# Performance work log

Hardware: AMD Instinct MI355X
Metric: run time of the kernel (lower is better)

Reference implementation:

```python
import jax, jax.numpy as jnp
import numpy as np

N_NODES = 100000
N_EDGES = 3200000
N_IN = 128
N_OUT = 64
ITERATIONS = 150
LEAK = 0.01


def _mml_activation(v):
    # piecewise: leaky below 0, Michaelis-Menten-like saturation above 0.5
    v = jnp.where(v < 0, v * LEAK, v)
    safe = jnp.where(v > 0.5, v, 1.0)  # avoid div-by-zero on untaken branch
    return jnp.where(v > 0.5, 1.0 - 0.25 / safe, v)


def setup_inputs() -> dict:
    key = jax.random.key(0)
    ks = jax.random.split(key, 9)
    x = jax.random.normal(ks[0], (1, N_IN), dtype=jnp.float32)
    in_weights = jnp.ones((N_IN,), jnp.float32)  # inputAmplitude * ones
    # weights init: 0.1 + 0.1*U, sign flipped for inhibitory reactions
    mag = 0.1 + 0.1 * jax.random.uniform(ks[1], (N_EDGES,), dtype=jnp.float32)
    sign = jnp.where(jax.random.bernoulli(ks[2], 0.5, (N_EDGES,)), 1.0, -1.0)
    rec_weights = mag * sign
    biases = 0.001 * jnp.ones((N_NODES,), jnp.float32)
    out_weights = jnp.ones((N_OUT,), jnp.float32)  # projectionAmplitude * ones
    in_indices = jax.random.randint(ks[3], (N_IN,), 0, N_NODES, dtype=jnp.int32)
    edge_rows = jax.random.randint(ks[4], (N_EDGES,), 0, N_NODES, dtype=jnp.int32)
    edge_cols = jax.random.randint(ks[5], (N_EDGES,), 0, N_NODES, dtype=jnp.int32)
    out_indices = jax.random.randint(ks[6], (N_OUT,), 0, N_NODES, dtype=jnp.int32)
    return {"x": x, "in_weights": in_weights, "rec_weights": rec_weights,
            "biases": biases, "out_weights": out_weights,
            "in_indices": in_indices, "edge_rows": edge_rows,
            "edge_cols": edge_cols, "out_indices": out_indices}


def reference(x, in_weights, rec_weights, biases, out_weights,
              in_indices, edge_rows, edge_cols, out_indices):
    # input projection: scatter weighted inputs into node vector [N_NODES]
    node_in = jnp.zeros((N_NODES,), x.dtype).at[in_indices].set(in_weights * x[0])
    b_in = node_in + biases

    def step(y, _):
        # sparse matvec A @ y: gather sources, weight, scatter-add to rows
        s = jax.ops.segment_sum(rec_weights * y[edge_cols], edge_rows,
                                num_segments=N_NODES)
        return _mml_activation(s + b_in), None

    y0 = jnp.zeros((N_NODES,), x.dtype)
    y, _ = jax.lax.scan(step, y0, None, length=ITERATIONS)
    # output projection: gather + scale -> [1, N_OUT]
    return (out_weights * y[out_indices])[None, :]
```

## Files before the change

kernel.cpp:

```cpp
#include <hip/hip_runtime.h>

#define N_NODES 100000
#define N_EDGES 3200000
#define N_IN    128
#define N_OUT   64
#define ITERS   150
#define LEAK    0.01f

#define NT      960
#define GROUPS  240
#define NBW     255
#define GRID    256
#define RPB2    393
#define NCH     9
#define CH      11520
#define CHF4    2880
#define NKEYS   (NCH * N_NODES)
#define SCAN_CHUNK 1024
#define SCAN_NBLK  879
#define NEPC    16
#define EPST    32
#define YSTR    (NCH * CH)

__device__ __forceinline__ float mml(float v) {
    v = (v < 0.0f) ? v * LEAK : v;
    if (v > 0.5f) v = 1.0f - 0.25f / v;
    return v;
}

__global__ void k_binit(const float* __restrict__ biases, float* __restrict__ b_in) {
    int i = blockIdx.x * blockDim.x + threadIdx.x;
    if (i < N_NODES) b_in[i] = biases[i];
}

__global__ void k_scatter_in(const float* __restrict__ x,
                             const float* __restrict__ in_w,
                             const int*   __restrict__ in_idx,
                             const float* __restrict__ biases,
                             float* __restrict__ b_in) {
    int k = threadIdx.x;
    if (k < N_IN) {
        int idx = in_idx[k];
        bool last = true;
        for (int j = k + 1; j < N_IN; ++j)
            if (in_idx[j] == idx) { last = false; break; }
        if (last) b_in[idx] = biases[idx] + in_w[k] * x[k];
    }
}

__global__ void k_y0(const float* __restrict__ b_in, float* __restrict__ y0) {
    int i = blockIdx.x * blockDim.x + threadIdx.x;
    if (i < N_NODES) y0[i] = mml(b_in[i]);
}

__global__ void k_hist(const int* __restrict__ rows, const int* __restrict__ cols,
                       int* __restrict__ counts) {
    int i = blockIdx.x * blockDim.x + threadIdx.x;
    int stride = gridDim.x * blockDim.x;
    for (; i < N_EDGES; i += stride) {
        int key = (cols[i] / CH) * N_NODES + rows[i];
        atomicAdd(&counts[key], 1);
    }
}

__global__ void k_scan1(const int* __restrict__ counts, int* __restrict__ rp,
                        int* __restrict__ blockSums) {
    __shared__ int sm[SCAN_CHUNK];
    int t = threadIdx.x;
    int i = blockIdx.x * SCAN_CHUNK + t;
    int v = (i < NKEYS) ? counts[i] : 0;
    sm[t] = v;
    __syncthreads();
    for (int off = 1; off < SCAN_CHUNK; off <<= 1) {
        int add = (t >= off) ? sm[t - off] : 0;
        __syncthreads();
        sm[t] += add;
        __syncthreads();
    }
    if (i <= NKEYS) rp[i] = sm[t] - v;
    if (t == SCAN_CHUNK - 1) blockSums[blockIdx.x] = sm[t];
}

__global__ void k_scan2(int* __restrict__ blockSums) {
    __shared__ int sm[1024];
    int t = threadIdx.x;
    int v = (t < SCAN_NBLK) ? blockSums[t] : 0;
    sm[t] = v;
    __syncthreads();
    for (int off = 1; off < 1024; off <<= 1) {
        int add = (t >= off) ? sm[t - off] : 0;
        __syncthreads();
        sm[t] += add;
        __syncthreads();
    }
    if (t < SCAN_NBLK) blockSums[t] = sm[t] - v;
}

__global__ void k_scan3(int* __restrict__ rp, const int* __restrict__ blockSums,
                        int* __restrict__ next) {
    int i = blockIdx.x * SCAN_CHUNK + threadIdx.x;
    if (i <= NKEYS) {
        int val = rp[i] + blockSums[blockIdx.x];
        rp[i] = val;
        if (i < NKEYS) next[i] = val;
    }
}

__global__ void k_scatter_edges(const int* __restrict__ rows, const int* __restrict__ cols,
                                const float* __restrict__ w,
                                int* __restrict__ next, int2* __restrict__ csr) {
    int i = blockIdx.x * blockDim.x + threadIdx.x;
    int stride = gridDim.x * blockDim.x;
    for (; i < N_EDGES; i += stride) {
        int c = cols[i];
        int g = c / CH;
        int key = g * N_NODES + rows[i];
        int p = atomicAdd(&next[key], 1);
        csr[p] = make_int2(c - g * CH, __float_as_int(w[i]));
    }
}

__device__ __forceinline__ void stage_chunk(const float* __restrict__ src,
                                            float* __restrict__ dst_lds,
                                            int t, int sc1mode) {
    if (!sc1mode) {
        #pragma unroll
        for (int i = 0; i < 3; ++i) {
            const int f4 = i * NT + t;
            __builtin_amdgcn_global_load_lds(
                (const __attribute__((address_space(1))) void*)(src + (size_t)f4 * 4),
                (__attribute__((address_space(3))) void*)(dst_lds + (size_t)f4 * 4),
                16, 0, 0);
        }
    } else {
        for (int i = t; i < CH; i += NT)
            dst_lds[i] = __hip_atomic_load(&src[i], __ATOMIC_RELAXED,
                                           __HIP_MEMORY_SCOPE_AGENT);
        asm volatile("s_waitcnt lgkmcnt(0)" ::: "memory");
    }
}

__device__ __forceinline__ void gate_poll(const int* __restrict__ epoch,
                                          int c, int need, int b) {
    while (__hip_atomic_load(&epoch[(c * NEPC + (b & (NEPC - 1))) * EPST],
                             __ATOMIC_RELAXED, __HIP_MEMORY_SCOPE_AGENT) < need)
        __builtin_amdgcn_s_sleep(1);
}

__global__ __launch_bounds__(NT) void k_iterate(
    const int*  __restrict__ rp2,
    const int2* __restrict__ csr,
    const float* __restrict__ b_in,
    float* __restrict__ ybufs,
    int* __restrict__ arr,
    int* __restrict__ epoch,
    const int* __restrict__ out_idx,
    const float* __restrict__ out_w,
    float* __restrict__ out,
    int nbuf, int sc1mode)
{
    __shared__ float sbufA[CH], sbufB[CH];
    __shared__ int   s_rp[NCH * 400];
    const int b = blockIdx.x, t = threadIdx.x;

    if (b == 0) {
        if (t < NCH * 64) {
            const int c = t >> 6, k = t & 63;
            int cend = (c + 1) * CH; if (cend > N_NODES) cend = N_NODES;
            const int wf = (c * CH) / RPB2;
            const int wl = (cend - 1) / RPB2;
            const int sz = wl - wf + 1;
            for (int v = 1; v <= ITERS - 1; ++v) {
                if (k < sz) {
                    while (__hip_atomic_load(&arr[1 + wf + k], __ATOMIC_RELAXED,
                                             __HIP_MEMORY_SCOPE_AGENT) < v)
                        __builtin_amdgcn_s_sleep(2);
                }
                if (k < NEPC)
                    __hip_atomic_store(&epoch[(c * NEPC + k) * EPST], v,
                                       __ATOMIC_RELAXED, __HIP_MEMORY_SCOPE_AGENT);
            }
        }
        return;
    }

    const int wi = b - 1;
    const int row0 = wi * RPB2;
    const int row_end = (row0 + RPB2 < N_NODES) ? row0 + RPB2 : N_NODES;
    const int nrows = row_end - row0;
    const int gq = t >> 2, j = t & 3;
    const int ord0 = ((row_end - 1) / CH + 1) % NCH;

    for (int c = 0; c < NCH; ++c)
        for (int i = t; i <= nrows; i += NT)
            s_rp[c * 400 + i] = rp2[(size_t)c * N_NODES + row0 + i];
    __syncthreads();

    stage_chunk(ybufs + (size_t)ord0 * CH, sbufA, t, sc1mode);

    for (int it = 1; it <= ITERS - 1; ++it) {
        const float* ysrc = ybufs + (size_t)((it - 1) % nbuf) * YSTR;
        float*       ydst = ybufs + (size_t)(it % nbuf) * YSTR;
        float acc1 = 0.f, acc2 = 0.f;

        for (int g = 0; g < NCH; ++g) {
            const int c = (ord0 + g) % NCH;
            if (g < NCH - 1) {
                const int cn = (ord0 + g + 1) % NCH;
                if (t == 0) gate_poll(epoch, cn, it - 1, b);
                __builtin_amdgcn_s_barrier();
                asm volatile("" ::: "memory");
                stage_chunk(ysrc + (size_t)cn * CH,
                            ((g + 1) & 1) ? sbufB : sbufA, t, sc1mode);
                asm volatile("s_waitcnt vmcnt(3)" ::: "memory");
            } else {
                asm volatile("s_waitcnt vmcnt(0)" ::: "memory");
            }
            __builtin_amdgcn_sched_barrier(0);
            __builtin_amdgcn_s_barrier();
            asm volatile("" ::: "memory");

            const float* __restrict__ sy = (g & 1) ? sbufB : sbufA;
            const int base = c * 400;
            if (gq < nrows) {
                int e = s_rp[base + gq] + j;
                const int end = s_rp[base + gq + 1];
                for (; e < end; e += 4) {
                    const int2 cc = csr[e];
                    acc1 += __int_as_float(cc.y) * sy[cc.x];
                }
            }
            if (gq + GROUPS < nrows) {
                int e = s_rp[base + gq + GROUPS] + j;
                const int end = s_rp[base + gq + GROUPS + 1];
                for (; e < end; e += 4) {
                    const int2 cc = csr[e];
                    acc2 += __int_as_float(cc.y) * sy[cc.x];
                }
            }
        }

        acc1 += __shfl_xor(acc1, 1); acc1 += __shfl_xor(acc1, 2);
        acc2 += __shfl_xor(acc2, 1); acc2 += __shfl_xor(acc2, 2);
        if (j == 0) {
            if (gq < nrows)
                __hip_atomic_store(&ydst[row0 + gq], mml(b_in[row0 + gq] + acc1),
                                   __ATOMIC_RELAXED, __HIP_MEMORY_SCOPE_AGENT);
            if (gq + GROUPS < nrows)
                __hip_atomic_store(&ydst[row0 + gq + GROUPS],
                                   mml(b_in[row0 + gq + GROUPS] + acc2),
                                   __ATOMIC_RELAXED, __HIP_MEMORY_SCOPE_AGENT);
        }
        asm volatile("s_waitcnt vmcnt(0)" ::: "memory");
        __builtin_amdgcn_s_barrier();
        if (t == 0)
            __hip_atomic_store(&arr[b], it, __ATOMIC_RELEASE,
                               __HIP_MEMORY_SCOPE_AGENT);

        if (it < ITERS - 1) {
            if (t == 0) gate_poll(epoch, ord0, it, b);
            __builtin_amdgcn_s_barrier();
            asm volatile("" ::: "memory");
            stage_chunk(ydst + (size_t)ord0 * CH, sbufA, t, sc1mode);
        }
    }

    if (b == 1) {
        if (t == 0)
            for (int c = 0; c < NCH; ++c)
                gate_poll(epoch, c, ITERS - 1, b);
        __syncthreads();
        if (t < N_OUT) {
            const float* yfin = ybufs + (size_t)((ITERS - 1) % nbuf) * YSTR;
            out[t] = out_w[t] * __hip_atomic_load(&yfin[out_idx[t]],
                       __ATOMIC_RELAXED, __HIP_MEMORY_SCOPE_AGENT);
        }
    }
}

extern "C" void kernel_launch(void* const* d_in, const int* in_sizes, int n_in,
                              void* d_out, int out_size, void* d_ws, size_t ws_size,
                              hipStream_t stream) {
    const float* x      = (const float*)d_in[0];
    const float* in_w   = (const float*)d_in[1];
    const float* rec_w  = (const float*)d_in[2];
    const float* biases = (const float*)d_in[3];
    const float* out_w  = (const float*)d_in[4];
    const int*   in_idx = (const int*)d_in[5];
    const int*   e_rows = (const int*)d_in[6];
    const int*   e_cols = (const int*)d_in[7];
    const int*   out_idx= (const int*)d_in[8];
    float* out = (float*)d_out;

    char* ws = (char*)d_ws;
    float* b_in    = (float*)ws;
    int*   rp2     = (int*)(b_in + N_NODES);
    int*   blockSums = rp2 + (NKEYS + 64);
    int*   arr     = blockSums + 1024;
    int*   epoch   = arr + 256;
    int*   counts  = epoch + NCH * NEPC * EPST;
    size_t off = (size_t)((char*)(counts + NKEYS) - ws);
    off = (off + 255) & ~(size_t)255;
    int2* csr = (int2*)(ws + off);
    size_t off2 = off + (size_t)N_EDGES * sizeof(int2);
    off2 = (off2 + 255) & ~(size_t)255;
    float* ybufs = (float*)(ws + off2);

    long long avail = ((long long)ws_size - (long long)off2) /
                      (long long)(YSTR * sizeof(float));
    int nbuf = (avail >= 150) ? 150 : (int)avail;
    int sc1mode = 0;
    if (nbuf < 40) { sc1mode = 1; if (nbuf > 4) nbuf = 4; }
    if (nbuf < 3) nbuf = 3;

    hipMemsetAsync(counts, 0, NKEYS * sizeof(int), stream);
    hipMemsetAsync(arr, 0, (256 + NCH * NEPC * EPST) * sizeof(int), stream);

    k_binit<<<391, 256, 0, stream>>>(biases, b_in);
    k_scatter_in<<<1, 128, 0, stream>>>(x, in_w, in_idx, biases, b_in);
    k_y0<<<391, 256, 0, stream>>>(b_in, ybufs);

    k_hist<<<1024, 256, 0, stream>>>(e_rows, e_cols, counts);
    k_scan1<<<SCAN_NBLK, SCAN_CHUNK, 0, stream>>>(counts, rp2, blockSums);
    k_scan2<<<1, 1024, 0, stream>>>(blockSums);
    k_scan3<<<SCAN_NBLK, SCAN_CHUNK, 0, stream>>>(rp2, blockSums, counts);
    k_scatter_edges<<<1024, 256, 0, stream>>>(e_rows, e_cols, rec_w, counts, csr);

    int*   rp_a   = rp2;
    int2*  csr_a  = csr;
    float* bin_a  = b_in;
    float* yb_a   = ybufs;
    int*   arr_a  = arr;
    int*   ep_a   = epoch;
    const int*   oidx_a = out_idx;
    const float* ow_a   = out_w;
    float* out_a  = out;
    void* args[] = { &rp_a, &csr_a, &bin_a, &yb_a, &arr_a, &ep_a,
                     &oidx_a, &ow_a, &out_a, &nbuf, &sc1mode };
    hipLaunchCooperativeKernel((void*)k_iterate, dim3(GRID), dim3(NT),
                               args, 0, stream);
}
```

Measured before the change: 3.295 ms.

## Replace per-chunk epoch gating with full grid barrier and triple-buffered chunk prefetch

Removes the dedicated coordinator block and the per-chunk epoch flags. Every block now does compute, and blocks meet at a grid-wide barrier each iteration, where all threads poll the per-block arrival counters (padded to separate cache lines). Chunks are staged into three LDS buffers with a prefetch distance of two, in a fixed order. This drops the coordinator latency and the fine-grained gating, but gives up overlapping the next iteration with blocks that are still working. The fallback path with few buffers is simplified to plain double buffering with synchronous loads.

```diff
diff --git a/kernel.cpp b/kernel.cpp
--- a/kernel.cpp
+++ b/kernel.cpp
@@ -7,20 +7,18 @@
 #define ITERS   150
 #define LEAK    0.01f
 
+#define NBLK    256
 #define NT      960
 #define GROUPS  240
-#define NBW     255
-#define GRID    256
-#define RPB2    393
+#define RPB     391
 #define NCH     9
 #define CH      11520
-#define CHF4    2880
 #define NKEYS   (NCH * N_NODES)
 #define SCAN_CHUNK 1024
 #define SCAN_NBLK  879
-#define NEPC    16
-#define EPST    32
+#define ARRSTR  16
 #define YSTR    (NCH * CH)
+#define NBUF    150
 
 __device__ __forceinline__ float mml(float v) {
     v = (v < 0.0f) ? v * LEAK : v;
@@ -121,30 +119,39 @@
 }
 
 __device__ __forceinline__ void stage_chunk(const float* __restrict__ src,
-                                            float* __restrict__ dst_lds,
-                                            int t, int sc1mode) {
-    if (!sc1mode) {
-        #pragma unroll
-        for (int i = 0; i < 3; ++i) {
-            const int f4 = i * NT + t;
-            __builtin_amdgcn_global_load_lds(
-                (const __attribute__((address_space(1))) void*)(src + (size_t)f4 * 4),
-                (__attribute__((address_space(3))) void*)(dst_lds + (size_t)f4 * 4),
-                16, 0, 0);
+                                            float* __restrict__ dst_lds, int t) {
+    #pragma unroll
+    for (int i = 0; i < 3; ++i) {
+        const int f4 = i * NT + t;
+        __builtin_amdgcn_global_load_lds(
+            (const __attribute__((address_space(1))) void*)(src + (size_t)f4 * 4),
+            (__attribute__((address_space(3))) void*)(dst_lds + (size_t)f4 * 4),
+            16, 0, 0);
+    }
+}
+
+__device__ __forceinline__ void chunk_compute(int c, const float* __restrict__ sy,
+                                              const int* __restrict__ s_rp,
+                                              const int2* __restrict__ csr,
+                                              int gq, int j, int nrows,
+                                              float& acc1, float& acc2) {
+    const int base = c * 392;
+    if (gq < nrows) {
+        int e = s_rp[base + gq] + j;
+        const int end = s_rp[base + gq + 1];
+        for (; e < end; e += 4) {
+            const int2 cc = csr[e];
+            acc1 += __int_as_float(cc.y) * sy[cc.x];
         }
-    } else {
-        for (int i = t; i < CH; i += NT)
-            dst_lds[i] = __hip_atomic_load(&src[i], __ATOMIC_RELAXED,
-                                           __HIP_MEMORY_SCOPE_AGENT);
-        asm volatile("s_waitcnt lgkmcnt(0)" ::: "memory");
-    }
-}
-
-__device__ __forceinline__ void gate_poll(const int* __restrict__ epoch,
-                                          int c, int need, int b) {
-    while (__hip_atomic_load(&epoch[(c * NEPC + (b & (NEPC - 1))) * EPST],
-                             __ATOMIC_RELAXED, __HIP_MEMORY_SCOPE_AGENT) < need)
-        __builtin_amdgcn_s_sleep(1);
+    }
+    if (gq + GROUPS < nrows) {
+        int e = s_rp[base + gq + GROUPS] + j;
+        const int end = s_rp[base + gq + GROUPS + 1];
+        for (; e < end; e += 4) {
+            const int2 cc = csr[e];
+            acc2 += __int_as_float(cc.y) * sy[cc.x];
+        }
+    }
 }
 
 __global__ __launch_bounds__(NT) void k_iterate(
@@ -153,128 +160,120 @@
     const float* __restrict__ b_in,
     float* __restrict__ ybufs,
     int* __restrict__ arr,
-    int* __restrict__ epoch,
     const int* __restrict__ out_idx,
     const float* __restrict__ out_w,
     float* __restrict__ out,
     int nbuf, int sc1mode)
 {
-    __shared__ float sbufA[CH], sbufB[CH];
-    __shared__ int   s_rp[NCH * 400];
+    __shared__ float sb0[CH], sb1[CH], sb2[CH];
+    __shared__ int s_rp[NCH * 392];
     const int b = blockIdx.x, t = threadIdx.x;
-
-    if (b == 0) {
-        if (t < NCH * 64) {
-            const int c = t >> 6, k = t & 63;
-            int cend = (c + 1) * CH; if (cend > N_NODES) cend = N_NODES;
-            const int wf = (c * CH) / RPB2;
-            const int wl = (cend - 1) / RPB2;
-            const int sz = wl - wf + 1;
-            for (int v = 1; v <= ITERS - 1; ++v) {
-                if (k < sz) {
-                    while (__hip_atomic_load(&arr[1 + wf + k], __ATOMIC_RELAXED,
-                                             __HIP_MEMORY_SCOPE_AGENT) < v)
-                        __builtin_amdgcn_s_sleep(2);
-                }
-                if (k < NEPC)
-                    __hip_atomic_store(&epoch[(c * NEPC + k) * EPST], v,
-                                       __ATOMIC_RELAXED, __HIP_MEMORY_SCOPE_AGENT);
-            }
-        }
-        return;
-    }
-
-    const int wi = b - 1;
-    const int row0 = wi * RPB2;
-    const int row_end = (row0 + RPB2 < N_NODES) ? row0 + RPB2 : N_NODES;
+    const int gq = t >> 2, j = t & 3;
+    const int row0 = b * RPB;
+    const int row_end = (row0 + RPB < N_NODES) ? row0 + RPB : N_NODES;
     const int nrows = row_end - row0;
-    const int gq = t >> 2, j = t & 3;
-    const int ord0 = ((row_end - 1) / CH + 1) % NCH;
 
     for (int c = 0; c < NCH; ++c)
         for (int i = t; i <= nrows; i += NT)
-            s_rp[c * 400 + i] = rp2[(size_t)c * N_NODES + row0 + i];
-    __syncthreads();
-
-    stage_chunk(ybufs + (size_t)ord0 * CH, sbufA, t, sc1mode);
-
-    for (int it = 1; it <= ITERS - 1; ++it) {
-        const float* ysrc = ybufs + (size_t)((it - 1) % nbuf) * YSTR;
-        float*       ydst = ybufs + (size_t)(it % nbuf) * YSTR;
-        float acc1 = 0.f, acc2 = 0.f;
-
-        for (int g = 0; g < NCH; ++g) {
-            const int c = (ord0 + g) % NCH;
-            if (g < NCH - 1) {
-                const int cn = (ord0 + g + 1) % NCH;
-                if (t == 0) gate_poll(epoch, cn, it - 1, b);
+            s_rp[c * 392 + i] = rp2[(size_t)c * N_NODES + row0 + i];
+
+    if (!sc1mode) {
+        stage_chunk(ybufs, sb0, t);
+        stage_chunk(ybufs + CH, sb1, t);
+        __syncthreads();
+
+        for (int it = 1; it <= ITERS - 1; ++it) {
+            const float* ysrc = ybufs + (size_t)((it - 1) % nbuf) * YSTR;
+            float*       ydst = ybufs + (size_t)(it % nbuf) * YSTR;
+            float acc1 = 0.f, acc2 = 0.f;
+
+            #pragma unroll
+            for (int g = 0; g < NCH; ++g) {
+                if (g < NCH - 1) asm volatile("s_waitcnt vmcnt(3)" ::: "memory");
+                else             asm volatile("s_waitcnt vmcnt(0)" ::: "memory");
                 __builtin_amdgcn_s_barrier();
-                asm volatile("" ::: "memory");
-                stage_chunk(ysrc + (size_t)cn * CH,
-                            ((g + 1) & 1) ? sbufB : sbufA, t, sc1mode);
-                asm volatile("s_waitcnt vmcnt(3)" ::: "memory");
-            } else {
-                asm volatile("s_waitcnt vmcnt(0)" ::: "memory");
-            }
-            __builtin_amdgcn_sched_barrier(0);
+                const float* sy = (g % 3 == 0) ? sb0 : (g % 3 == 1) ? sb1 : sb2;
+                chunk_compute(g, sy, s_rp, csr, gq, j, nrows, acc1, acc2);
+                if (g + 2 < NCH) {
+                    float* dst = ((g + 2) % 3 == 0) ? sb0 : ((g + 2) % 3 == 1) ? sb1 : sb2;
+                    stage_chunk(ysrc + (size_t)(g + 2) * CH, dst, t);
+                }
+            }
+
+            acc1 += __shfl_xor(acc1, 1); acc1 += __shfl_xor(acc1, 2);
+            acc2 += __shfl_xor(acc2, 1); acc2 += __shfl_xor(acc2, 2);
+            if (j == 0) {
+                if (gq < nrows)
+                    __hip_atomic_store(&ydst[row0 + gq], mml(b_in[row0 + gq] + acc1),
+                                       __ATOMIC_RELAXED, __HIP_MEMORY_SCOPE_AGENT);
+                if (gq + GROUPS < nrows)
+                    __hip_atomic_store(&ydst[row0 + gq + GROUPS],
+                                       mml(b_in[row0 + gq + GROUPS] + acc2),
+                                       __ATOMIC_RELAXED, __HIP_MEMORY_SCOPE_AGENT);
+            }
+            asm volatile("s_waitcnt vmcnt(0)" ::: "memory");
             __builtin_amdgcn_s_barrier();
-            asm volatile("" ::: "memory");
-
-            const float* __restrict__ sy = (g & 1) ? sbufB : sbufA;
-            const int base = c * 400;
-            if (gq < nrows) {
-                int e = s_rp[base + gq] + j;
-                const int end = s_rp[base + gq + 1];
-                for (; e < end; e += 4) {
-                    const int2 cc = csr[e];
-                    acc1 += __int_as_float(cc.y) * sy[cc.x];
-                }
-            }
-            if (gq + GROUPS < nrows) {
-                int e = s_rp[base + gq + GROUPS] + j;
-                const int end = s_rp[base + gq + GROUPS + 1];
-                for (; e < end; e += 4) {
-                    const int2 cc = csr[e];
-                    acc2 += __int_as_float(cc.y) * sy[cc.x];
-                }
+            if (t == 0)
+                __hip_atomic_store(&arr[b * ARRSTR], it, __ATOMIC_RELEASE,
+                                   __HIP_MEMORY_SCOPE_AGENT);
+            int ok;
+            do {
+                ok = 1;
+                if (t < NBLK)
+                    ok = (__hip_atomic_load(&arr[t * ARRSTR], __ATOMIC_RELAXED,
+                                            __HIP_MEMORY_SCOPE_AGENT) >= it);
+                if (!ok) __builtin_amdgcn_s_sleep(1);
+            } while (!__syncthreads_and(ok));
+
+            if (it < ITERS - 1) {
+                stage_chunk(ydst, sb0, t);
+                stage_chunk(ydst + CH, sb1, t);
             }
         }
-
-        acc1 += __shfl_xor(acc1, 1); acc1 += __shfl_xor(acc1, 2);
-        acc2 += __shfl_xor(acc2, 1); acc2 += __shfl_xor(acc2, 2);
-        if (j == 0) {
-            if (gq < nrows)
-                __hip_atomic_store(&ydst[row0 + gq], mml(b_in[row0 + gq] + acc1),
-                                   __ATOMIC_RELAXED, __HIP_MEMORY_SCOPE_AGENT);
-            if (gq + GROUPS < nrows)
-                __hip_atomic_store(&ydst[row0 + gq + GROUPS],
-                                   mml(b_in[row0 + gq + GROUPS] + acc2),
-                                   __ATOMIC_RELAXED, __HIP_MEMORY_SCOPE_AGENT);
+    } else {
+        __syncthreads();
+        for (int it = 1; it <= ITERS - 1; ++it) {
+            const float* ysrc = ybufs + (size_t)((it - 1) & 1) * YSTR;
+            float*       ydst = ybufs + (size_t)(it & 1) * YSTR;
+            float acc1 = 0.f, acc2 = 0.f;
+            for (int g = 0; g < NCH; ++g) {
+                for (int i = t; i < CH; i += NT)
+                    sb0[i] = __hip_atomic_load(&ysrc[(size_t)g * CH + i],
+                                               __ATOMIC_RELAXED, __HIP_MEMORY_SCOPE_AGENT);
+                __syncthreads();
+                chunk_compute(g, sb0, s_rp, csr, gq, j, nrows, acc1, acc2);
+                __syncthreads();
+            }
+            acc1 += __shfl_xor(acc1, 1); acc1 += __shfl_xor(acc1, 2);
+            acc2 += __shfl_xor(acc2, 1); acc2 += __shfl_xor(acc2, 2);
+            if (j == 0) {
+                if (gq < nrows)
+                    __hip_atomic_store(&ydst[row0 + gq], mml(b_in[row0 + gq] + acc1),
+                                       __ATOMIC_RELAXED, __HIP_MEMORY_SCOPE_AGENT);
+                if (gq + GROUPS < nrows)
+                    __hip_atomic_store(&ydst[row0 + gq + GROUPS],
+                                       mml(b_in[row0 + gq + GROUPS] + acc2),
+                                       __ATOMIC_RELAXED, __HIP_MEMORY_SCOPE_AGENT);
+            }
+            __syncthreads();
+            if (t == 0)
+                __hip_atomic_store(&arr[b * ARRSTR], it, __ATOMIC_RELEASE,
+                                   __HIP_MEMORY_SCOPE_AGENT);
+            int ok;
+            do {
+                ok = 1;
+                if (t < NBLK)
+                    ok = (__hip_atomic_load(&arr[t * ARRSTR], __ATOMIC_RELAXED,
+                                            __HIP_MEMORY_SCOPE_AGENT) >= it);
+                if (!ok) __builtin_amdgcn_s_sleep(1);
+            } while (!__syncthreads_and(ok));
         }
-        asm volatile("s_waitcnt vmcnt(0)" ::: "memory");
-        __builtin_amdgcn_s_barrier();
-        if (t == 0)
-            __hip_atomic_store(&arr[b], it, __ATOMIC_RELEASE,
-                               __HIP_MEMORY_SCOPE_AGENT);
-
-        if (it < ITERS - 1) {
-            if (t == 0) gate_poll(epoch, ord0, it, b);
-            __builtin_amdgcn_s_barrier();
-            asm volatile("" ::: "memory");
-            stage_chunk(ydst + (size_t)ord0 * CH, sbufA, t, sc1mode);
-        }
-    }
-
-    if (b == 1) {
-        if (t == 0)
-            for (int c = 0; c < NCH; ++c)
-                gate_poll(epoch, c, ITERS - 1, b);
-        __syncthreads();
-        if (t < N_OUT) {
-            const float* yfin = ybufs + (size_t)((ITERS - 1) % nbuf) * YSTR;
-            out[t] = out_w[t] * __hip_atomic_load(&yfin[out_idx[t]],
-                       __ATOMIC_RELAXED, __HIP_MEMORY_SCOPE_AGENT);
-        }
+    }
+
+    if (b == 0 && t < N_OUT) {
+        const float* yfin = ybufs + (size_t)((ITERS - 1) % nbuf) * YSTR;
+        out[t] = out_w[t] * __hip_atomic_load(&yfin[out_idx[t]],
+                   __ATOMIC_RELAXED, __HIP_MEMORY_SCOPE_AGENT);
     }
 }
 
@@ -297,8 +296,7 @@
     int*   rp2     = (int*)(b_in + N_NODES);
     int*   blockSums = rp2 + (NKEYS + 64);
     int*   arr     = blockSums + 1024;
-    int*   epoch   = arr + 256;
-    int*   counts  = epoch + NCH * NEPC * EPST;
+    int*   counts  = arr + NBLK * ARRSTR;
     size_t off = (size_t)((char*)(counts + NKEYS) - ws);
     off = (off + 255) & ~(size_t)255;
     int2* csr = (int2*)(ws + off);
@@ -308,13 +306,12 @@
 
     long long avail = ((long long)ws_size - (long long)off2) /
                       (long long)(YSTR * sizeof(float));
-    int nbuf = (avail >= 150) ? 150 : (int)avail;
-    int sc1mode = 0;
-    if (nbuf < 40) { sc1mode = 1; if (nbuf > 4) nbuf = 4; }
-    if (nbuf < 3) nbuf = 3;
+    int nbuf, sc1mode;
+    if (avail >= NBUF) { nbuf = NBUF; sc1mode = 0; }
+    else               { nbuf = 2;    sc1mode = 1; }
 
     hipMemsetAsync(counts, 0, NKEYS * sizeof(int), stream);
-    hipMemsetAsync(arr, 0, (256 + NCH * NEPC * EPST) * sizeof(int), stream);
+    hipMemsetAsync(arr, 0, NBLK * ARRSTR * sizeof(int), stream);
 
     k_binit<<<391, 256, 0, stream>>>(biases, b_in);
     k_scatter_in<<<1, 128, 0, stream>>>(x, in_w, in_idx, biases, b_in);
@@ -331,12 +328,11 @@
     float* bin_a  = b_in;
     float* yb_a   = ybufs;
     int*   arr_a  = arr;
-    int*   ep_a   = epoch;
     const int*   oidx_a = out_idx;
     const float* ow_a   = out_w;
     float* out_a  = out;
-    void* args[] = { &rp_a, &csr_a, &bin_a, &yb_a, &arr_a, &ep_a,
+    void* args[] = { &rp_a, &csr_a, &bin_a, &yb_a, &arr_a,
                      &oidx_a, &ow_a, &out_a, &nbuf, &sc1mode };
-    hipLaunchCooperativeKernel((void*)k_iterate, dim3(GRID), dim3(NT),
+    hipLaunchCooperativeKernel((void*)k_iterate, dim3(NBLK), dim3(NT),
                                args, 0, stream);
 }
```

Result: faster. 3.204 ms (-2.8%).
